# Kernel tuning notes

Hardware: AMD Instinct MI355X
Metric: run time of the kernel (lower is better)

## Reference

```python
import jax, jax.numpy as jnp
import numpy as np


def _bit_reversal_perm(N, num_stages):
    idx = np.arange(N)
    perm = np.zeros(N, dtype=np.int64)
    for _ in range(num_stages):
        perm = (perm << 1) | (idx & 1)
        idx >>= 1
    return perm


def setup_inputs() -> dict:
    key = jax.random.key(0)
    k1, k2 = jax.random.split(key)
    B, N = 4096, 4096
    return {
        "x_re": jax.random.normal(k1, (B, N), dtype=jnp.float32),
        "x_im": jax.random.normal(k2, (B, N), dtype=jnp.float32),
    }


def reference(x_re, x_im):
    # Radix-2 DIT FFT, identical math to HollywoodFFT.forward.
    N = x_re.shape[-1]
    num_stages = int(round(np.log2(N)))
    batch = x_re.shape[:-1]

    # Input permutation is pure wiring: bit-reversal gather.
    perm = jnp.asarray(_bit_reversal_perm(N, num_stages))
    y_re = x_re[..., perm]
    y_im = x_im[..., perm]

    # Twiddle tile: W_N^k = exp(-2*pi*i*k/N) (precomputed constants).
    k = np.arange(N)
    ang = -2.0 * np.pi * k / N
    W_re_all = np.cos(ang).astype(np.float32)
    W_im_all = np.sin(ang).astype(np.float32)

    for s in range(num_stages):  # fixed small loop over log2(N) stages
        stride = 1 << s
        group_size = stride << 1
        # twiddle_idx = j * (N // group_size) for j in [0, stride), same for every group
        tw = np.arange(stride) * (N // group_size)
        W_re = jnp.asarray(W_re_all[tw])  # (stride,)
        W_im = jnp.asarray(W_im_all[tw])

        # (..., N) -> (..., N//group_size, 2, stride): [...,g,0,j]=upper, [...,g,1,j]=lower
        yr = y_re.reshape(*batch, N // group_size, 2, stride)
        yi = y_im.reshape(*batch, N // group_size, 2, stride)
        a_re, b_re = yr[..., 0, :], yr[..., 1, :]
        a_im, b_im = yi[..., 0, :], yi[..., 1, :]

        wb_re = W_re * b_re - W_im * b_im
        wb_im = W_re * b_im + W_im * b_re

        y_re = jnp.stack([a_re + wb_re, a_re - wb_re], axis=-2).reshape(*batch, N)
        y_im = jnp.stack([a_im + wb_im, a_im - wb_im], axis=-2).reshape(*batch, N)

    return y_re, y_im
```

## Files before the change

### kernel.cpp

```cpp
#include <hip/hip_runtime.h>


#define NFFT 4096

__device__ __forceinline__ void fft16(float xr[16], float xi[16]) {
    const int br[16] = {0,8,4,12,2,10,6,14,1,9,5,13,3,11,7,15};
    float yr[16], yi[16];
#pragma unroll
    for (int j = 0; j < 16; ++j) { yr[j] = xr[br[j]]; yi[j] = xi[br[j]]; }
    const float W16r[8] = { 1.0f,  0.92387953251128675613f,  0.70710678118654752440f,
                            0.38268343236508977173f,  0.0f, -0.38268343236508977173f,
                           -0.70710678118654752440f, -0.92387953251128675613f };
    const float W16i[8] = { 0.0f, -0.38268343236508977173f, -0.70710678118654752440f,
                           -0.92387953251128675613f, -1.0f, -0.92387953251128675613f,
                           -0.70710678118654752440f, -0.38268343236508977173f };
#pragma unroll
    for (int s = 0; s < 4; ++s) {
        const int stride = 1 << s;
        const int tm = 8 >> s;
#pragma unroll
        for (int g = 0; g < 16; g += 2 * stride) {
#pragma unroll
            for (int p = 0; p < stride; ++p) {
                const int i0 = g + p, i1 = i0 + stride;
                const float twr = W16r[p * tm], twi = W16i[p * tm];
                const float brr = yr[i1] * twr - yi[i1] * twi;
                const float bii = yr[i1] * twi + yi[i1] * twr;
                const float ar = yr[i0], ai = yi[i0];
                yr[i0] = ar + brr; yi[i0] = ai + bii;
                yr[i1] = ar - brr; yi[i1] = ai - bii;
            }
        }
    }
#pragma unroll
    for (int j = 0; j < 16; ++j) { xr[j] = yr[j]; xi[j] = yi[j]; }
}

__global__ __launch_bounds__(256, 4)
void HollywoodFFT_53584011985637_kernel(const float* __restrict__ xre,
                                        const float* __restrict__ xim,
                                        float* __restrict__ outre,
                                        float* __restrict__ outim) {
    __shared__ float lr[4368];
    __shared__ float li[4368];

    const int t = threadIdx.x;
    const long long row = blockIdx.x;
    const float* __restrict__ xr_row = xre + row * NFFT;
    const float* __restrict__ xi_row = xim + row * NFFT;

    float vr[16], vi[16];
    const int a = t & 15;
#pragma unroll
    for (int c = 0; c < 16; ++c) {
        vr[c] = xr_row[t + 256 * c];
        vi[c] = xi_row[t + 256 * c];
    }
    fft16(vr, vi);
#pragma unroll
    for (int u = 0; u < 16; ++u) {
        lr[t + 264 * u] = vr[u];
        li[t + 264 * u] = vi[u];
    }
    __syncthreads();

    const int u = t >> 4;
    {
        float s0, c0;
        __sincosf(-6.28318530717958647692f * (float)u * (1.0f / 256.0f), &s0, &c0);
        float twr = 1.0f, twi = 0.0f;
#pragma unroll
        for (int bb = 0; bb < 16; ++bb) {
            const int id = a + 16 * bb + 264 * u;
            const float rr = lr[id], ii = li[id];
            vr[bb] = rr * twr - ii * twi;
            vi[bb] = rr * twi + ii * twr;
            const float ntr = twr * c0 - twi * s0;
            twi = twr * s0 + twi * c0;
            twr = ntr;
        }
    }
    __syncthreads();
    fft16(vr, vi);
#pragma unroll
    for (int v = 0; v < 16; ++v) {
        lr[2 * a + 17 * u + 272 * v] = vr[v];
        li[2 * a + 17 * u + 272 * v] = vi[v];
    }
    __syncthreads();

    const int u2 = t & 15, v2 = t >> 4;
    {
        float s0, c0;
        __sincosf(-6.28318530717958647692f * (float)(u2 + 16 * v2) * (1.0f / 4096.0f),
                  &s0, &c0);
        float twr = 1.0f, twi = 0.0f;
#pragma unroll
        for (int aa = 0; aa < 16; ++aa) {
            const int id = 2 * aa + 17 * u2 + 272 * v2;
            const float rr = lr[id], ii = li[id];
            vr[aa] = rr * twr - ii * twi;
            vi[aa] = rr * twi + ii * twr;
            const float ntr = twr * c0 - twi * s0;
            twi = twr * s0 + twi * c0;
            twr = ntr;
        }
    }
    fft16(vr, vi);

    float* __restrict__ or_row = outre + row * NFFT;
    float* __restrict__ oi_row = outim + row * NFFT;
#pragma unroll
    for (int w = 0; w < 16; ++w) {
        or_row[t + 256 * w] = vr[w];
        oi_row[t + 256 * w] = vi[w];
    }
}

extern "C" void kernel_launch(void* const* d_in, const int* in_sizes, int n_in,
                              void* d_out, int out_size, void* d_ws, size_t ws_size,
                              hipStream_t stream) {
    const float* xre = (const float*)d_in[0];
    const float* xim = (const float*)d_in[1];
    const int B = in_sizes[0] / NFFT;
    float* out = (float*)d_out;
    float* outre = out;
    float* outim = out + (size_t)B * NFFT;
    HollywoodFFT_53584011985637_kernel<<<dim3(B), dim3(256), 0, stream>>>(
        xre, xim, outre, outim);
}
```

Measured before the change: 238.0 us.

## Stage global I/O through LDS with 128-bit loads/stores and XOR-swizzled layout

```diff
diff --git a/kernel.cpp b/kernel.cpp
--- a/kernel.cpp
+++ b/kernel.cpp
@@ -2,6 +2,8 @@
 
 
 #define NFFT 4096
+
+typedef float fvec4 __attribute__((ext_vector_type(4)));
 
 __device__ __forceinline__ void fft16(float xr[16], float xi[16]) {
     const int br[16] = {0,8,4,12,2,10,6,14,1,9,5,13,3,11,7,15};
@@ -36,42 +38,55 @@
     for (int j = 0; j < 16; ++j) { xr[j] = yr[j]; xi[j] = yi[j]; }
 }
 
-__global__ __launch_bounds__(256, 4)
+__global__ __launch_bounds__(256, 5)
 void HollywoodFFT_53584011985637_kernel(const float* __restrict__ xre,
                                         const float* __restrict__ xim,
                                         float* __restrict__ outre,
                                         float* __restrict__ outim) {
-    __shared__ float lr[4368];
-    __shared__ float li[4368];
+    __shared__ __align__(16) float lr[NFFT];
+    __shared__ __align__(16) float li[NFFT];
 
     const int t = threadIdx.x;
     const long long row = blockIdx.x;
     const float* __restrict__ xr_row = xre + row * NFFT;
     const float* __restrict__ xi_row = xim + row * NFFT;
 
-    float vr[16], vi[16];
-    const int a = t & 15;
+    {
+        const fvec4* __restrict__ xr4 = (const fvec4*)xr_row;
+        const fvec4* __restrict__ xi4 = (const fvec4*)xi_row;
+        fvec4 rr[4], ii[4];
 #pragma unroll
-    for (int c = 0; c < 16; ++c) {
-        vr[c] = xr_row[t + 256 * c];
-        vi[c] = xi_row[t + 256 * c];
-    }
-    fft16(vr, vi);
+        for (int q = 0; q < 4; ++q) { rr[q] = xr4[t + 256 * q]; ii[q] = xi4[t + 256 * q]; }
 #pragma unroll
-    for (int u = 0; u < 16; ++u) {
-        lr[t + 264 * u] = vr[u];
-        li[t + 264 * u] = vi[u];
+        for (int q = 0; q < 4; ++q) {
+            ((fvec4*)lr)[t + 256 * q] = rr[q];
+            ((fvec4*)li)[t + 256 * q] = ii[q];
+        }
     }
     __syncthreads();
 
+    float vr[16], vi[16];
+    const int a = t & 15;
     const int u = t >> 4;
+
+#pragma unroll
+    for (int c = 0; c < 16; ++c) { vr[c] = lr[t + 256 * c]; vi[c] = li[t + 256 * c]; }
+    fft16(vr, vi);
+    __syncthreads();
+#pragma unroll
+    for (int uu = 0; uu < 16; ++uu) {
+        const int id = a + 16 * ((t >> 4) ^ uu) + 256 * uu;
+        lr[id] = vr[uu]; li[id] = vi[uu];
+    }
+    __syncthreads();
+
     {
         float s0, c0;
         __sincosf(-6.28318530717958647692f * (float)u * (1.0f / 256.0f), &s0, &c0);
         float twr = 1.0f, twi = 0.0f;
 #pragma unroll
         for (int bb = 0; bb < 16; ++bb) {
-            const int id = a + 16 * bb + 264 * u;
+            const int id = a + 16 * (bb ^ u) + 256 * u;
             const float rr = lr[id], ii = li[id];
             vr[bb] = rr * twr - ii * twi;
             vi[bb] = rr * twi + ii * twr;
@@ -80,12 +95,12 @@
             twr = ntr;
         }
     }
+    fft16(vr, vi);
     __syncthreads();
-    fft16(vr, vi);
 #pragma unroll
     for (int v = 0; v < 16; ++v) {
-        lr[2 * a + 17 * u + 272 * v] = vr[v];
-        li[2 * a + 17 * u + 272 * v] = vi[v];
+        const int id = (a ^ u) + 16 * (u ^ v) + 256 * v;
+        lr[id] = vr[v]; li[id] = vi[v];
     }
     __syncthreads();
 
@@ -97,7 +112,7 @@
         float twr = 1.0f, twi = 0.0f;
 #pragma unroll
         for (int aa = 0; aa < 16; ++aa) {
-            const int id = 2 * aa + 17 * u2 + 272 * v2;
+            const int id = (aa ^ u2) + 16 * (u2 ^ v2) + 256 * v2;
             const float rr = lr[id], ii = li[id];
             vr[aa] = rr * twr - ii * twi;
             vi[aa] = rr * twi + ii * twr;
@@ -107,13 +122,24 @@
         }
     }
     fft16(vr, vi);
-
-    float* __restrict__ or_row = outre + row * NFFT;
-    float* __restrict__ oi_row = outim + row * NFFT;
+    __syncthreads();
 #pragma unroll
     for (int w = 0; w < 16; ++w) {
-        or_row[t + 256 * w] = vr[w];
-        oi_row[t + 256 * w] = vi[w];
+        const int id = u2 + 16 * v2 + 256 * w;
+        lr[id] = vr[w]; li[id] = vi[w];
+    }
+    __syncthreads();
+
+    {
+        float* __restrict__ or_row = outre + row * NFFT;
+        float* __restrict__ oi_row = outim + row * NFFT;
+#pragma unroll
+        for (int q = 0; q < 4; ++q) {
+            fvec4 rr = ((const fvec4*)lr)[t + 256 * q];
+            fvec4 ii = ((const fvec4*)li)[t + 256 * q];
+            __builtin_nontemporal_store(rr, (fvec4*)or_row + t + 256 * q);
+            __builtin_nontemporal_store(ii, (fvec4*)oi_row + t + 256 * q);
+        }
     }
 }
 
```

New measurement: 235.4 us. About the same (-1.1%).
